# Performance work log

Hardware: AMD Instinct MI355X
Metric: run time of the kernel (lower is better)

The kernel has to match this reference:

```python
import jax, jax.numpy as jnp
import numpy as np

B, S, D = 64, 2048, 64

def setup_inputs() -> dict:
    key = jax.random.key(0)
    k1, k2, k3, k4 = jax.random.split(key, 4)
    query = jax.random.normal(k1, (B, S, D), dtype=jnp.float32)
    keyt = jax.random.normal(k2, (B, S, D), dtype=jnp.float32)
    value = jax.random.normal(k3, (B, S, D), dtype=jnp.float32)
    mask = jax.random.randint(k4, (1, S, S), 0, 2, dtype=jnp.int32)
    return {"query": query, "key": keyt, "value": value, "mask": mask}

def reference(query, key, value, mask):
    # scores: [B, S, S]
    scale = jnp.sqrt(jnp.asarray(value.shape[-1], dtype=query.dtype))
    scores = jnp.einsum('bqd,bkd->bqk', query, key) / scale
    scores = jnp.where(mask == 0, jnp.asarray(-1e9, dtype=scores.dtype), scores)
    attention_weights = jax.nn.softmax(scores, axis=-1)
    # dropout p=0.0 -> identity
    context = jnp.einsum('bqk,bkd->bqd', attention_weights, value)
    return (context, attention_weights)
```

## Files before the change

### kernel.cpp

```cpp
#include <hip/hip_runtime.h>

#define NB 64
#define NS 2048
#define ND 64
#define KSTEP 64
#define NIT (NS / KSTEP)

typedef __bf16 bf16x8 __attribute__((ext_vector_type(8)));
typedef float f32x4 __attribute__((ext_vector_type(4)));
typedef unsigned int u32;
typedef u32 u32x2 __attribute__((ext_vector_type(2)));
typedef u32 u32x4 __attribute__((ext_vector_type(4)));
typedef unsigned short u16;
typedef u16 u16x8 __attribute__((ext_vector_type(8)));

#define C2F 0.18033688011112042f

__device__ __forceinline__ float fexp2(float x) { return exp2f(x); }
__device__ __forceinline__ float flog2(float x) { return log2f(x); }

#define TILE_BARRIER()                                   \
  do {                                                   \
    asm volatile("s_waitcnt lgkmcnt(0)" ::: "memory");   \
    __builtin_amdgcn_s_barrier();                        \
    asm volatile("" ::: "memory");                       \
  } while (0)

__device__ __forceinline__ u16 f2bs(float x) {
  __bf16 h = (__bf16)x;
  return __builtin_bit_cast(u16, h);
}

__device__ __forceinline__ bf16x8 cvt8(f32x4 a, f32x4 b) {
  bf16x8 r;
  r[0] = (__bf16)a[0]; r[1] = (__bf16)a[1]; r[2] = (__bf16)a[2]; r[3] = (__bf16)a[3];
  r[4] = (__bf16)b[0]; r[5] = (__bf16)b[1]; r[6] = (__bf16)b[2]; r[7] = (__bf16)b[3];
  return r;
}

__global__ __launch_bounds__(256) void prep_cast_k(const float* __restrict__ K,
                                                   u16* __restrict__ Kbf) {
  const size_t i = ((size_t)blockIdx.x * 256 + threadIdx.x) * 8;
  f32x4 a = __builtin_nontemporal_load((const f32x4*)(K + i));
  f32x4 b = __builtin_nontemporal_load((const f32x4*)(K + i + 4));
  *(bf16x8*)(Kbf + i) = cvt8(a, b);
}

__global__ __launch_bounds__(256) void prep_transp_v(const float* __restrict__ V,
                                                     u16* __restrict__ VT) {
  __shared__ __attribute__((aligned(16))) u16 T[64][72];
  const int b = blockIdx.x >> 5, kt = blockIdx.x & 31;
  const float* src = V + ((size_t)b * NS + kt * 64) * ND;
  {
    const int k = threadIdx.x >> 2, d0 = (threadIdx.x & 3) * 16;
    const float* p = src + (size_t)k * ND + d0;
    f32x4 a0 = __builtin_nontemporal_load((const f32x4*)p);
    f32x4 a1 = __builtin_nontemporal_load((const f32x4*)(p + 4));
    f32x4 a2 = __builtin_nontemporal_load((const f32x4*)(p + 8));
    f32x4 a3 = __builtin_nontemporal_load((const f32x4*)(p + 12));
    *(bf16x8*)&T[k][d0]     = cvt8(a0, a1);
    *(bf16x8*)&T[k][d0 + 8] = cvt8(a2, a3);
  }
  __syncthreads();
  const int d = threadIdx.x >> 2, k0 = (threadIdx.x & 3) * 16;
  u16x8 r0, r1;
#pragma unroll
  for (int j = 0; j < 8; ++j) {
    const int P0 = k0 + j, P1 = k0 + 8 + j;
    const int s0 = 32 * (P0 >> 5) + 16 * ((P0 >> 2) & 1) + 4 * ((P0 >> 3) & 3) + (P0 & 3);
    const int s1 = 32 * (P1 >> 5) + 16 * ((P1 >> 2) & 1) + 4 * ((P1 >> 3) & 3) + (P1 & 3);
    r0[j] = T[s0][d];
    r1[j] = T[s1][d];
  }
  u16* dst = VT + ((size_t)b * ND + d) * NS + kt * 64 + k0;
  *(u16x8*)dst = r0;
  *(u16x8*)(dst + 8) = r1;
}

__global__ __launch_bounds__(256) void prep_pack_mask(const int* __restrict__ M,
                                                      unsigned long long* __restrict__ Mb) {
  const size_t i = (size_t)blockIdx.x * 256 + threadIdx.x;
  const unsigned long long bal = __ballot(M[i] != 0);
  if ((threadIdx.x & 63) == 0) Mb[i >> 6] = bal;
}

template <bool PRE>
__global__ __launch_bounds__(512, 4) void DotProductAttention_22436909154804_kernel(
    const float* __restrict__ Q, const float* __restrict__ K,
    const float* __restrict__ V, const int* __restrict__ M,
    const u16* __restrict__ Kbf, const u16* __restrict__ VTbf,
    const u32* __restrict__ Mb, float* __restrict__ ctx, float* __restrict__ wts) {
  __shared__ __attribute__((aligned(16))) u16 Kt[2][64][72];
  __shared__ __attribute__((aligned(16))) u16 Vt[2][64][72];
  __shared__ float Rs[2][64];

  const int tid  = threadIdx.x;
  const int lane = tid & 63;
  const int w    = tid >> 6;
  const int wq   = w & 3;
  const int kt   = w >> 2;
  const int g    = lane >> 4;
  const int c    = lane & 15;

  const int bid = blockIdx.x;
  const int vb  = (bid & 7) * 256 + (bid >> 3);
  const int b   = vb >> 5;
  const int qt  = vb & 31;
  const int q0w = qt * 64 + wq * 16;
  const size_t bq = (size_t)b * NS;

  const float* qp = Q + (bq + q0w + c) * ND + 8 * g;
  f32x4 qa = __builtin_nontemporal_load((const f32x4*)qp);
  f32x4 qb = __builtin_nontemporal_load((const f32x4*)(qp + 4));
  const bf16x8 qf0 = cvt8(qa, qb);
  qa = __builtin_nontemporal_load((const f32x4*)(qp + 32));
  qb = __builtin_nontemporal_load((const f32x4*)(qp + 36));
  const bf16x8 qf1 = cvt8(qa, qb);

  const u16* Kbb = PRE ? (Kbf + bq * ND) : (const u16*)nullptr;
  const u16* VTb = PRE ? (VTbf + bq * ND) : (const u16*)nullptr;
  const float* Kb32 = K + bq * ND;
  const float* Vb32 = V + bq * ND;
  const int* Mr   = M + (size_t)(q0w + c) * NS + kt * 32;
  const u32* MbRow = Mb + (size_t)(q0w + c) * (NS / 32);
  const u32* Mbr   = MbRow + kt;

  const bool isK = tid < 256;
  const int st   = tid & 255;

  auto msel = [](float e, u32 mm, int idx) -> float {
    u32 keep = (u32)(((int)(mm << (31 - idx))) >> 31);
    return __uint_as_float(__float_as_uint(e) & keep);
  };

  const f32x4 zz = {0.f, 0.f, 0.f, 0.f};
  float rs = 0.f;

  if (PRE) {
    const int r1  = tid >> 2;
    const int cc1 = (tid & 3) * 16;
    u16x8 pa, pb;
    auto issueP1 = [&](int kb) {
      const u16* p = Kbb + (size_t)(kb + r1) * ND + cc1;
      pa = *(const u16x8*)p;
      pb = *(const u16x8*)(p + 8);
    };
    auto writeP1 = [&](int pair) {
      u16(*dst)[72] = pair ? Vt[r1 >> 6] : Kt[r1 >> 6];
      *(u16x8*)&dst[r1 & 63][cc1]     = pa;
      *(u16x8*)&dst[r1 & 63][cc1 + 8] = pb;
    };
    issueP1(0);
    writeP1(0);
    __syncthreads();
    for (int it = 0; it < 16; ++it) {
      const int pair = it & 1;
      if (it + 1 < 16) issueP1((it + 1) * 128);
      const u32x2 mv = *(const u32x2*)(MbRow + it * 4 + kt * 2);
      u16(*B)[72] = pair ? Vt[kt] : Kt[kt];
#pragma unroll
      for (int j = 0; j < 4; ++j) {
        bf16x8 a0 = *(const bf16x8*)&B[16 * j + c][8 * g];
        bf16x8 a1 = *(const bf16x8*)&B[16 * j + c][32 + 8 * g];
        f32x4 s = __builtin_amdgcn_mfma_f32_16x16x32_bf16(a0, qf0, zz, 0, 0, 0);
        s = __builtin_amdgcn_mfma_f32_16x16x32_bf16(a1, qf1, s, 0, 0, 0);
        const u32 mm = (j < 2) ? mv.x : mv.y;
        const int base = 16 * (j & 1) + 4 * g;
        rs += msel(fexp2(s[0] * C2F), mm, base + 0)
            + msel(fexp2(s[1] * C2F), mm, base + 1)
            + msel(fexp2(s[2] * C2F), mm, base + 2)
            + msel(fexp2(s[3] * C2F), mm, base + 3);
      }
      if (it + 1 < 16) writeP1((it + 1) & 1);
      TILE_BARRIER();
    }
  } else {
    f32x4 kf0, kf1, kf2, kf3;
    auto issueK1 = [&](int kb) {
      if (isK) {
        const int r = st >> 2, cc = (st & 3) * 16;
        const float* p = Kb32 + (size_t)(kb + r) * ND + cc;
        kf0 = *(const f32x4*)p;       kf1 = *(const f32x4*)(p + 4);
        kf2 = *(const f32x4*)(p + 8); kf3 = *(const f32x4*)(p + 12);
      }
    };
    auto writeK1 = [&](int buf) {
      if (isK) {
        const int r = st >> 2, cc = (st & 3) * 16;
        *(bf16x8*)&Kt[buf][r][cc]     = cvt8(kf0, kf1);
        *(bf16x8*)&Kt[buf][r][cc + 8] = cvt8(kf2, kf3);
      }
    };
    issueK1(0);
    writeK1(0);
    __syncthreads();
    for (int it = 0; it < NIT; ++it) {
      const int cur = it & 1, kb = it * KSTEP;
      if (it + 1 < NIT) issueK1(kb + KSTEP);
#pragma unroll
      for (int j = 0; j < 2; ++j) {
        bf16x8 a0 = *(const bf16x8*)&Kt[cur][kt * 32 + 16 * j + c][8 * g];
        bf16x8 a1 = *(const bf16x8*)&Kt[cur][kt * 32 + 16 * j + c][32 + 8 * g];
        f32x4 s = __builtin_amdgcn_mfma_f32_16x16x32_bf16(a0, qf0, zz, 0, 0, 0);
        s = __builtin_amdgcn_mfma_f32_16x16x32_bf16(a1, qf1, s, 0, 0, 0);
        const int4 m4 = *(const int4*)(Mr + kb + 16 * j + 4 * g);
        rs += (m4.x ? fexp2(s[0] * C2F) : 0.f)
            + (m4.y ? fexp2(s[1] * C2F) : 0.f)
            + (m4.z ? fexp2(s[2] * C2F) : 0.f)
            + (m4.w ? fexp2(s[3] * C2F) : 0.f);
      }
      if (it + 1 < NIT) writeK1((it + 1) & 1);
      TILE_BARRIER();
    }
  }
  rs += __shfl_xor(rs, 16);
  rs += __shfl_xor(rs, 32);

  u16x8 sp0, sp1;
  f32x4 kf0, kf1, kf2, kf3;
  auto issueKV = [&](int kb) {
    if (PRE) {
      if (isK) {
        const int r = st >> 2, cc = (st & 3) * 16;
        const u16* p = Kbb + (size_t)(kb + r) * ND + cc;
        sp0 = *(const u16x8*)p; sp1 = *(const u16x8*)(p + 8);
      } else {
        const int d = st >> 2, kc = (st & 3) * 16;
        const u16* p = VTb + (size_t)d * NS + kb + kc;
        sp0 = *(const u16x8*)p; sp1 = *(const u16x8*)(p + 8);
      }
    } else {
      if (isK) {
        const int r = st >> 2, cc = (st & 3) * 16;
        const float* p = Kb32 + (size_t)(kb + r) * ND + cc;
        kf0 = *(const f32x4*)p;       kf1 = *(const f32x4*)(p + 4);
        kf2 = *(const f32x4*)(p + 8); kf3 = *(const f32x4*)(p + 12);
      } else {
        const int k = st >> 2, d0 = (st & 3) * 16;
        const float* p = Vb32 + (size_t)(kb + k) * ND + d0;
        kf0 = *(const f32x4*)p;       kf1 = *(const f32x4*)(p + 4);
        kf2 = *(const f32x4*)(p + 8); kf3 = *(const f32x4*)(p + 12);
      }
    }
  };
  auto writeKV = [&](int buf) {
    if (PRE) {
      if (isK) {
        const int r = st >> 2, cc = (st & 3) * 16;
        *(u16x8*)&Kt[buf][r][cc] = sp0; *(u16x8*)&Kt[buf][r][cc + 8] = sp1;
      } else {
        const int d = st >> 2, kc = (st & 3) * 16;
        *(u16x8*)&Vt[buf][d][kc] = sp0; *(u16x8*)&Vt[buf][d][kc + 8] = sp1;
      }
    } else {
      if (isK) {
        const int r = st >> 2, cc = (st & 3) * 16;
        *(bf16x8*)&Kt[buf][r][cc]     = cvt8(kf0, kf1);
        *(bf16x8*)&Kt[buf][r][cc + 8] = cvt8(kf2, kf3);
      } else {
        const int k = st >> 2, d0 = (st & 3) * 16;
        bf16x8 v0 = cvt8(kf0, kf1), v1 = cvt8(kf2, kf3);
#pragma unroll
        for (int j = 0; j < 8; ++j) {
          Vt[buf][d0 + j][k]     = __builtin_bit_cast(u16, v0[j]);
          Vt[buf][d0 + 8 + j][k] = __builtin_bit_cast(u16, v1[j]);
        }
      }
    }
  };

  issueKV(0);
  if (lane < 16) Rs[kt][wq * 16 + c] = rs;
  __syncthreads();
  const float l2inv = -flog2(Rs[0][wq * 16 + c] + Rs[1][wq * 16 + c]);
  writeKV(0);
  __syncthreads();

  f32x4 acc[4] = {zz, zz, zz, zz};
  float* wrow = wts + (bq + q0w + c) * NS + kt * 32;
  for (int it = 0; it < NIT; ++it) {
    const int cur = it & 1, kb = it * KSTEP;
    if (it + 1 < NIT) issueKV(kb + KSTEP);
    u32 mm = 0;
    if (PRE) mm = Mbr[kb >> 5];

    u32 wpk[4];
#pragma unroll
    for (int j = 0; j < 2; ++j) {
      bf16x8 a0 = *(const bf16x8*)&Kt[cur][kt * 32 + 16 * j + c][8 * g];
      bf16x8 a1 = *(const bf16x8*)&Kt[cur][kt * 32 + 16 * j + c][32 + 8 * g];
      f32x4 s = __builtin_amdgcn_mfma_f32_16x16x32_bf16(a0, qf0, zz, 0, 0, 0);
      s = __builtin_amdgcn_mfma_f32_16x16x32_bf16(a1, qf1, s, 0, 0, 0);
      float w0, w1, w2, w3;
      if (PRE) {
        w0 = msel(fexp2(fmaf(s[0], C2F, l2inv)), mm, 16 * j + 4 * g + 0);
        w1 = msel(fexp2(fmaf(s[1], C2F, l2inv)), mm, 16 * j + 4 * g + 1);
        w2 = msel(fexp2(fmaf(s[2], C2F, l2inv)), mm, 16 * j + 4 * g + 2);
        w3 = msel(fexp2(fmaf(s[3], C2F, l2inv)), mm, 16 * j + 4 * g + 3);
      } else {
        const int4 m4 = *(const int4*)(Mr + kb + 16 * j + 4 * g);
        w0 = m4.x ? fexp2(fmaf(s[0], C2F, l2inv)) : 0.f;
        w1 = m4.y ? fexp2(fmaf(s[1], C2F, l2inv)) : 0.f;
        w2 = m4.z ? fexp2(fmaf(s[2], C2F, l2inv)) : 0.f;
        w3 = m4.w ? fexp2(fmaf(s[3], C2F, l2inv)) : 0.f;
      }
      f32x4 wv = {w0, w1, w2, w3};
      __builtin_nontemporal_store(wv, (f32x4*)(wrow + kb + 16 * j + 4 * g));
      wpk[2 * j]     = (u32)f2bs(w0) | ((u32)f2bs(w1) << 16);
      wpk[2 * j + 1] = (u32)f2bs(w2) | ((u32)f2bs(w3) << 16);
    }

    u32x4 wu = {wpk[0], wpk[1], wpk[2], wpk[3]};
    bf16x8 wb = __builtin_bit_cast(bf16x8, wu);
#pragma unroll
    for (int dt = 0; dt < 4; ++dt) {
      bf16x8 va;
      if (PRE) {
        va = *(const bf16x8*)&Vt[cur][dt * 16 + c][kt * 32 + 8 * g];
      } else {
        u32x2 vlo = *(const u32x2*)&Vt[cur][dt * 16 + c][kt * 32 + 4 * g];
        u32x2 vhi = *(const u32x2*)&Vt[cur][dt * 16 + c][kt * 32 + 16 + 4 * g];
        u32x4 vau = {vlo.x, vlo.y, vhi.x, vhi.y};
        va = __builtin_bit_cast(bf16x8, vau);
      }
      acc[dt] = __builtin_amdgcn_mfma_f32_16x16x32_bf16(va, wb, acc[dt], 0, 0, 0);
    }

    if (it + 1 < NIT) writeKV((it + 1) & 1);
    TILE_BARRIER();
  }

  float* red = (float*)&Kt[0][0][0] + wq * 1088;
  if (kt == 1) {
#pragma unroll
    for (int dt = 0; dt < 4; ++dt)
      *(f32x4*)&red[c * 68 + dt * 16 + 4 * g] = acc[dt];
  }
  __syncthreads();
  if (kt == 0) {
    float* crow = ctx + (bq + q0w + c) * ND;
#pragma unroll
    for (int dt = 0; dt < 4; ++dt) {
      f32x4 vv = acc[dt] + *(const f32x4*)&red[c * 68 + dt * 16 + 4 * g];
      __builtin_nontemporal_store(vv, (f32x4*)(crow + dt * 16 + 4 * g));
    }
  }
}

extern "C" void kernel_launch(void* const* d_in, const int* in_sizes, int n_in,
                              void* d_out, int out_size, void* d_ws, size_t ws_size,
                              hipStream_t stream) {
  const float* Q = (const float*)d_in[0];
  const float* K = (const float*)d_in[1];
  const float* V = (const float*)d_in[2];
  const int*   M = (const int*)d_in[3];
  float* ctx = (float*)d_out;
  float* wts = (float*)d_out + (size_t)NB * NS * ND;

  dim3 grid(NB * (NS / 64));
  dim3 block(512);

  constexpr size_t KBF_B = (size_t)NB * NS * ND * 2;
  constexpr size_t MB_B  = (size_t)NS * NS / 8;
  u16* Kbf = (u16*)d_ws;
  u16* VTb = (u16*)((char*)d_ws + KBF_B);
  unsigned long long* Mb64 = (unsigned long long*)((char*)d_ws + 2 * KBF_B);

  if (ws_size >= 2 * KBF_B + MB_B) {
    hipLaunchKernelGGL(prep_cast_k, dim3(NB * NS * ND / 8 / 256), dim3(256), 0, stream, K, Kbf);
    hipLaunchKernelGGL(prep_transp_v, dim3(NB * (NS / 64)), dim3(256), 0, stream, V, VTb);
    hipLaunchKernelGGL(prep_pack_mask, dim3(NS * NS / 256), dim3(256), 0, stream, M, Mb64);
    hipLaunchKernelGGL(DotProductAttention_22436909154804_kernel<true>, grid, block, 0, stream,
                       Q, K, V, M, Kbf, VTb, (const u32*)Mb64, ctx, wts);
  } else {
    hipLaunchKernelGGL(DotProductAttention_22436909154804_kernel<false>, grid, block, 0, stream,
                       Q, K, V, M, (const u16*)nullptr, (const u16*)nullptr,
                       (const u32*)nullptr, ctx, wts);
  }
}
```

Baseline: 347.2 us.

## Fuse prep kernels into one launch, vectorize mask packing, relax occupancy bound

Merges the three preprocessing kernels (K cast, V transpose, mask bit-pack) into a single launch that dispatches on block index. Mask packing now has each thread read 32 ints as vector loads and build one u32, instead of a wave ballot over scalar loads. The main kernel's launch_bounds minimum-blocks hint drops from 4 to 3, giving the compiler more registers. The row-sum accumulation is split into two partial sums, and several __syncthreads become explicit lgkmcnt waits plus barriers. The change saves launch overhead and may reduce spilling, at the risk of lower occupancy.

```diff
diff --git a/kernel.cpp b/kernel.cpp
--- a/kernel.cpp
+++ b/kernel.cpp
@@ -13,6 +13,7 @@
 typedef u32 u32x4 __attribute__((ext_vector_type(4)));
 typedef unsigned short u16;
 typedef u16 u16x8 __attribute__((ext_vector_type(8)));
+typedef int i32x4 __attribute__((ext_vector_type(4)));
 
 #define C2F 0.18033688011112042f
 
@@ -38,54 +39,65 @@
   return r;
 }
 
-__global__ __launch_bounds__(256) void prep_cast_k(const float* __restrict__ K,
-                                                   u16* __restrict__ Kbf) {
-  const size_t i = ((size_t)blockIdx.x * 256 + threadIdx.x) * 8;
-  f32x4 a = __builtin_nontemporal_load((const f32x4*)(K + i));
-  f32x4 b = __builtin_nontemporal_load((const f32x4*)(K + i + 4));
-  *(bf16x8*)(Kbf + i) = cvt8(a, b);
-}
-
-__global__ __launch_bounds__(256) void prep_transp_v(const float* __restrict__ V,
-                                                     u16* __restrict__ VT) {
+__global__ __launch_bounds__(256) void prep_fused(const float* __restrict__ K,
+                                                  const float* __restrict__ V,
+                                                  const int* __restrict__ M,
+                                                  u16* __restrict__ Kbf,
+                                                  u16* __restrict__ VT,
+                                                  u32* __restrict__ Mb) {
   __shared__ __attribute__((aligned(16))) u16 T[64][72];
-  const int b = blockIdx.x >> 5, kt = blockIdx.x & 31;
-  const float* src = V + ((size_t)b * NS + kt * 64) * ND;
-  {
-    const int k = threadIdx.x >> 2, d0 = (threadIdx.x & 3) * 16;
-    const float* p = src + (size_t)k * ND + d0;
-    f32x4 a0 = __builtin_nontemporal_load((const f32x4*)p);
-    f32x4 a1 = __builtin_nontemporal_load((const f32x4*)(p + 4));
-    f32x4 a2 = __builtin_nontemporal_load((const f32x4*)(p + 8));
-    f32x4 a3 = __builtin_nontemporal_load((const f32x4*)(p + 12));
-    *(bf16x8*)&T[k][d0]     = cvt8(a0, a1);
-    *(bf16x8*)&T[k][d0 + 8] = cvt8(a2, a3);
-  }
-  __syncthreads();
-  const int d = threadIdx.x >> 2, k0 = (threadIdx.x & 3) * 16;
-  u16x8 r0, r1;
-#pragma unroll
-  for (int j = 0; j < 8; ++j) {
-    const int P0 = k0 + j, P1 = k0 + 8 + j;
-    const int s0 = 32 * (P0 >> 5) + 16 * ((P0 >> 2) & 1) + 4 * ((P0 >> 3) & 3) + (P0 & 3);
-    const int s1 = 32 * (P1 >> 5) + 16 * ((P1 >> 2) & 1) + 4 * ((P1 >> 3) & 3) + (P1 & 3);
-    r0[j] = T[s0][d];
-    r1[j] = T[s1][d];
-  }
-  u16* dst = VT + ((size_t)b * ND + d) * NS + kt * 64 + k0;
-  *(u16x8*)dst = r0;
-  *(u16x8*)(dst + 8) = r1;
-}
-
-__global__ __launch_bounds__(256) void prep_pack_mask(const int* __restrict__ M,
-                                                      unsigned long long* __restrict__ Mb) {
-  const size_t i = (size_t)blockIdx.x * 256 + threadIdx.x;
-  const unsigned long long bal = __ballot(M[i] != 0);
-  if ((threadIdx.x & 63) == 0) Mb[i >> 6] = bal;
+  const int bid = blockIdx.x;
+  if (bid < 4096) {
+    const size_t i = ((size_t)bid * 256 + threadIdx.x) * 8;
+    f32x4 a = __builtin_nontemporal_load((const f32x4*)(K + i));
+    f32x4 b = __builtin_nontemporal_load((const f32x4*)(K + i + 4));
+    *(bf16x8*)(Kbf + i) = cvt8(a, b);
+  } else if (bid < 6144) {
+    const int vbid = bid - 4096;
+    const int b = vbid >> 5, kt = vbid & 31;
+    const float* src = V + ((size_t)b * NS + kt * 64) * ND;
+    {
+      const int k = threadIdx.x >> 2, d0 = (threadIdx.x & 3) * 16;
+      const float* p = src + (size_t)k * ND + d0;
+      f32x4 a0 = __builtin_nontemporal_load((const f32x4*)p);
+      f32x4 a1 = __builtin_nontemporal_load((const f32x4*)(p + 4));
+      f32x4 a2 = __builtin_nontemporal_load((const f32x4*)(p + 8));
+      f32x4 a3 = __builtin_nontemporal_load((const f32x4*)(p + 12));
+      *(bf16x8*)&T[k][d0]     = cvt8(a0, a1);
+      *(bf16x8*)&T[k][d0 + 8] = cvt8(a2, a3);
+    }
+    __syncthreads();
+    const int d = threadIdx.x >> 2, k0 = (threadIdx.x & 3) * 16;
+    u16x8 r0, r1;
+#pragma unroll
+    for (int j = 0; j < 8; ++j) {
+      const int P0 = k0 + j, P1 = k0 + 8 + j;
+      const int s0 = 32 * (P0 >> 5) + 16 * ((P0 >> 2) & 1) + 4 * ((P0 >> 3) & 3) + (P0 & 3);
+      const int s1 = 32 * (P1 >> 5) + 16 * ((P1 >> 2) & 1) + 4 * ((P1 >> 3) & 3) + (P1 & 3);
+      r0[j] = T[s0][d];
+      r1[j] = T[s1][d];
+    }
+    u16* dst = VT + ((size_t)b * ND + d) * NS + kt * 64 + k0;
+    *(u16x8*)dst = r0;
+    *(u16x8*)(dst + 8) = r1;
+  } else {
+    const int tg = (bid - 6144) * 256 + threadIdx.x;
+    const i32x4* p = (const i32x4*)(M + (size_t)tg * 32);
+    u32 bits = 0;
+#pragma unroll
+    for (int j = 0; j < 8; ++j) {
+      i32x4 m = p[j];
+      bits |= (u32)(m[0] != 0) << (4 * j);
+      bits |= (u32)(m[1] != 0) << (4 * j + 1);
+      bits |= (u32)(m[2] != 0) << (4 * j + 2);
+      bits |= (u32)(m[3] != 0) << (4 * j + 3);
+    }
+    Mb[tg] = bits;
+  }
 }
 
 template <bool PRE>
-__global__ __launch_bounds__(512, 4) void DotProductAttention_22436909154804_kernel(
+__global__ __launch_bounds__(512, 3) void DotProductAttention_22436909154804_kernel(
     const float* __restrict__ Q, const float* __restrict__ K,
     const float* __restrict__ V, const int* __restrict__ M,
     const u16* __restrict__ Kbf, const u16* __restrict__ VTbf,
@@ -134,7 +146,7 @@
   };
 
   const f32x4 zz = {0.f, 0.f, 0.f, 0.f};
-  float rs = 0.f;
+  float rs0 = 0.f, rs1 = 0.f;
 
   if (PRE) {
     const int r1  = tid >> 2;
@@ -166,10 +178,12 @@
         s = __builtin_amdgcn_mfma_f32_16x16x32_bf16(a1, qf1, s, 0, 0, 0);
         const u32 mm = (j < 2) ? mv.x : mv.y;
         const int base = 16 * (j & 1) + 4 * g;
-        rs += msel(fexp2(s[0] * C2F), mm, base + 0)
-            + msel(fexp2(s[1] * C2F), mm, base + 1)
-            + msel(fexp2(s[2] * C2F), mm, base + 2)
-            + msel(fexp2(s[3] * C2F), mm, base + 3);
+        float t0 = msel(fexp2(s[0] * C2F), mm, base + 0)
+                 + msel(fexp2(s[1] * C2F), mm, base + 1);
+        float t1 = msel(fexp2(s[2] * C2F), mm, base + 2)
+                 + msel(fexp2(s[3] * C2F), mm, base + 3);
+        rs0 += t0;
+        rs1 += t1;
       }
       if (it + 1 < 16) writeP1((it + 1) & 1);
       TILE_BARRIER();
@@ -204,15 +218,16 @@
         f32x4 s = __builtin_amdgcn_mfma_f32_16x16x32_bf16(a0, qf0, zz, 0, 0, 0);
         s = __builtin_amdgcn_mfma_f32_16x16x32_bf16(a1, qf1, s, 0, 0, 0);
         const int4 m4 = *(const int4*)(Mr + kb + 16 * j + 4 * g);
-        rs += (m4.x ? fexp2(s[0] * C2F) : 0.f)
-            + (m4.y ? fexp2(s[1] * C2F) : 0.f)
-            + (m4.z ? fexp2(s[2] * C2F) : 0.f)
-            + (m4.w ? fexp2(s[3] * C2F) : 0.f);
+        rs0 += (m4.x ? fexp2(s[0] * C2F) : 0.f)
+             + (m4.y ? fexp2(s[1] * C2F) : 0.f);
+        rs1 += (m4.z ? fexp2(s[2] * C2F) : 0.f)
+             + (m4.w ? fexp2(s[3] * C2F) : 0.f);
       }
       if (it + 1 < NIT) writeK1((it + 1) & 1);
       TILE_BARRIER();
     }
   }
+  float rs = rs0 + rs1;
   rs += __shfl_xor(rs, 16);
   rs += __shfl_xor(rs, 32);
 
@@ -271,10 +286,10 @@
 
   issueKV(0);
   if (lane < 16) Rs[kt][wq * 16 + c] = rs;
-  __syncthreads();
+  TILE_BARRIER();
   const float l2inv = -flog2(Rs[0][wq * 16 + c] + Rs[1][wq * 16 + c]);
   writeKV(0);
-  __syncthreads();
+  TILE_BARRIER();
 
   f32x4 acc[4] = {zz, zz, zz, zz};
   float* wrow = wts + (bq + q0w + c) * NS + kt * 32;
@@ -336,7 +351,7 @@
     for (int dt = 0; dt < 4; ++dt)
       *(f32x4*)&red[c * 68 + dt * 16 + 4 * g] = acc[dt];
   }
-  __syncthreads();
+  TILE_BARRIER();
   if (kt == 0) {
     float* crow = ctx + (bq + q0w + c) * ND;
 #pragma unroll
@@ -364,14 +379,12 @@
   constexpr size_t MB_B  = (size_t)NS * NS / 8;
   u16* Kbf = (u16*)d_ws;
   u16* VTb = (u16*)((char*)d_ws + KBF_B);
-  unsigned long long* Mb64 = (unsigned long long*)((char*)d_ws + 2 * KBF_B);
+  u32* Mb32 = (u32*)((char*)d_ws + 2 * KBF_B);
 
   if (ws_size >= 2 * KBF_B + MB_B) {
-    hipLaunchKernelGGL(prep_cast_k, dim3(NB * NS * ND / 8 / 256), dim3(256), 0, stream, K, Kbf);
-    hipLaunchKernelGGL(prep_transp_v, dim3(NB * (NS / 64)), dim3(256), 0, stream, V, VTb);
-    hipLaunchKernelGGL(prep_pack_mask, dim3(NS * NS / 256), dim3(256), 0, stream, M, Mb64);
+    hipLaunchKernelGGL(prep_fused, dim3(6656), dim3(256), 0, stream, K, V, M, Kbf, VTb, Mb32);
     hipLaunchKernelGGL(DotProductAttention_22436909154804_kernel<true>, grid, block, 0, stream,
-                       Q, K, V, M, Kbf, VTb, (const u32*)Mb64, ctx, wts);
+                       Q, K, V, M, Kbf, VTb, Mb32, ctx, wts);
   } else {
     hipLaunchKernelGGL(DotProductAttention_22436909154804_kernel<false>, grid, block, 0, stream,
                        Q, K, V, M, (const u16*)nullptr, (const u16*)nullptr,
```

Result: no change. 349.6 us (+0.7%).
